# Kernel tuning notes

Hardware: AMD Instinct MI355X
Metric: run time of the kernel (lower is better)

The kernel has to match this reference:

```python
import jax, jax.numpy as jnp
import numpy as np

B, S, D, H = 2, 4096, 1024, 16
HD = D // H  # 64


def setup_inputs() -> dict:
    key = jax.random.key(0)
    ks = jax.random.split(key, 9)
    init = lambda k, shape: (jax.random.normal(k, shape, dtype=jnp.float32) * 0.02)
    return {
        "x": jax.random.normal(ks[0], (B, S, D), dtype=jnp.float32),
        "Wq": init(ks[1], (D, D)), "bq": init(ks[2], (D,)),
        "Wk": init(ks[3], (D, D)), "bk": init(ks[4], (D,)),
        "Wv": init(ks[5], (D, D)), "bv": init(ks[6], (D,)),
        "Wo": init(ks[7], (D, D)), "bo": init(ks[8], (D,)),
    }


def _split_heads(t):
    # [B, S, D] -> [B, H, S, HD]
    b, s, d = t.shape
    return t.reshape(b, s, H, HD).transpose(0, 2, 1, 3)


def reference(x, Wq, bq, Wk, bk, Wv, bv, Wo, bo):
    # q/k/v projections (torch Linear: x @ W.T + b)
    q = _split_heads(x @ Wq.T + bq)
    k = _split_heads(x @ Wk.T + bk)
    v = _split_heads(x @ Wv.T + bv)
    scale = 1.0 / np.sqrt(HD).astype(np.float32)
    # chunked_attention uses full K/V per chunk => equivalent to full attention.
    scores = jnp.einsum("bhqd,bhkd->bhqk", q, k) * scale
    # softmax computed in fp32 then cast back (matches F.softmax(dtype=float32))
    attn = jax.nn.softmax(scores.astype(jnp.float32), axis=-1).astype(scores.dtype)
    out = jnp.einsum("bhqk,bhkd->bhqd", attn, v)
    out = out.transpose(0, 2, 1, 3).reshape(B, S, D)  # combine heads
    return out @ Wo.T + bo
```

## Files before the change

### kernel.cpp

```cpp
#include <hip/hip_runtime.h>
#include <hip/hip_bf16.h>
#include <stdint.h>

typedef __attribute__((ext_vector_type(8))) short short8;
typedef __attribute__((ext_vector_type(4))) short short4v;
typedef __attribute__((ext_vector_type(4))) float f32x4;
typedef __attribute__((ext_vector_type(4))) unsigned int uint4v;

#define MFMA16(A, B, C) __builtin_amdgcn_mfma_f32_16x16x32_bf16(A, B, C, 0, 0, 0)

#define GLDS16(gp, lp) __builtin_amdgcn_global_load_lds(                     \
    (const __attribute__((address_space(1))) unsigned int*)(gp),             \
    (__attribute__((address_space(3))) unsigned int*)(lp), 16, 0, 0)

static constexpr int kS  = 4096;
static constexpr int kD  = 1024;
static constexpr int kH  = 16;
static constexpr int kHD = 64;

__device__ __forceinline__ short bf16_bits(float f) {
    __hip_bfloat16 h = __float2bfloat16(f);
    return *(short*)&h;
}

__device__ __forceinline__ unsigned int pk_bf16(float a, float b) {
    __hip_bfloat162 h = __float22bfloat162_rn(make_float2(a, b));
    return *(unsigned int*)&h;
}

__device__ __forceinline__ short8 cvt8(const float* __restrict__ p) {
    f32x4 a = ((const f32x4*)p)[0];
    f32x4 b = ((const f32x4*)p)[1];
    short8 r;
    r[0] = bf16_bits(a[0]); r[1] = bf16_bits(a[1]);
    r[2] = bf16_bits(a[2]); r[3] = bf16_bits(a[3]);
    r[4] = bf16_bits(b[0]); r[5] = bf16_bits(b[1]);
    r[6] = bf16_bits(b[2]); r[7] = bf16_bits(b[3]);
    return r;
}

__device__ __forceinline__ unsigned char f32_to_e4m3(float f) {
    unsigned int u = __float_as_uint(f);
    unsigned int s = (u >> 24) & 0x80u;
    unsigned int a = u & 0x7fffffffu;
    if (a < 0x3c800000u) {
        float af = __uint_as_float(a);
        unsigned int sub = (unsigned int)(af * 512.0f + 0.5f);
        return (unsigned char)(s | sub);
    }
    unsigned int r = a + 0x80000u;
    unsigned int m = (r >> 20) & 7u;
    int eb = (int)(r >> 23) - 127 + 7;
    unsigned int bits = ((unsigned int)eb << 3) | m;
    if (bits > 0x7Eu) bits = 0x7Eu;
    return (unsigned char)(s | bits);
}
__device__ __forceinline__ float e4m3_to_f32(unsigned int b) {
    unsigned int s = b & 0x80u;
    unsigned int e = (b >> 3) & 15u;
    unsigned int m = b & 7u;
    float f = e ? __uint_as_float(((e + 120u) << 23) | (m << 20))
                : (float)m * 0.001953125f;
    return s ? -f : f;
}

__global__ __launch_bounds__(256) void cvt_f32_bf16(
    const float* __restrict__ src, __hip_bfloat16* __restrict__ dst)
{
    const int i = blockIdx.x * 256 + threadIdx.x;
    f32x4 v = ((const f32x4*)src)[i];
    short4v o;
    o[0] = bf16_bits(v[0]); o[1] = bf16_bits(v[1]);
    o[2] = bf16_bits(v[2]); o[3] = bf16_bits(v[3]);
    ((short4v*)dst)[i] = o;
}

__global__ __launch_bounds__(256) void cvt_w4(
    const float* __restrict__ w0, const float* __restrict__ w1,
    const float* __restrict__ w2, const float* __restrict__ w3,
    __hip_bfloat16* __restrict__ dst)
{
    const int blk = blockIdx.x;
    const int sel = blk >> 10;
    const float* src = sel == 0 ? w0 : sel == 1 ? w1 : sel == 2 ? w2 : w3;
    const int i = (blk & 1023) * 256 + threadIdx.x;
    f32x4 v = ((const f32x4*)src)[i];
    short4v o;
    o[0] = bf16_bits(v[0]); o[1] = bf16_bits(v[1]);
    o[2] = bf16_bits(v[2]); o[3] = bf16_bits(v[3]);
    ((short4v*)(dst + (size_t)sel * kD * kD))[i] = o;
}

__global__ __launch_bounds__(256) void cvt_all(
    const float* __restrict__ x,
    const float* __restrict__ w0, const float* __restrict__ w1,
    const float* __restrict__ w2, const float* __restrict__ w3,
    __hip_bfloat16* __restrict__ xb, __hip_bfloat16* __restrict__ wdst)
{
    int blk = blockIdx.x;
    const float* src;
    __hip_bfloat16* dst;
    int i;
    if (blk < 8192) {
        src = x; dst = xb; i = blk * 256 + threadIdx.x;
    } else {
        blk -= 8192;
        const int sel = blk >> 10;
        src = sel == 0 ? w0 : sel == 1 ? w1 : sel == 2 ? w2 : w3;
        dst = wdst + (size_t)sel * kD * kD;
        i = (blk & 1023) * 256 + threadIdx.x;
    }
    f32x4 v = ((const f32x4*)src)[i];
    short4v o;
    o[0] = bf16_bits(v[0]); o[1] = bf16_bits(v[1]);
    o[2] = bf16_bits(v[2]); o[3] = bf16_bits(v[3]);
    ((short4v*)dst)[i] = o;
}


__global__ __launch_bounds__(256) void gemm_qkv(
    const __hip_bfloat16* __restrict__ X, const __hip_bfloat16* __restrict__ Wb,
    const float* __restrict__ bq, const float* __restrict__ bk,
    const float* __restrict__ bv,
    __hip_bfloat16* __restrict__ Qw, __hip_bfloat16* __restrict__ Kw,
    __hip_bfloat16* __restrict__ Vtw)
{
    __shared__ short As[128 * 64];
    __shared__ short Bs[128 * 64];

    const int lane = threadIdx.x & 63, wave = threadIdx.x >> 6;
    const int quad = lane >> 4, l16 = lane & 15;
    const int sel = blockIdx.y >> 3;
    const int m0 = blockIdx.x * 128, n0 = (blockIdx.y & 7) * 128;
    const int wm = wave & 1, wn = wave >> 1;

    const float* bias = sel == 0 ? bq : sel == 1 ? bk : bv;
    const short* Xg = (const short*)X + (size_t)m0 * kD;
    const short* Wg = (const short*)Wb + (size_t)sel * kD * kD + (size_t)n0 * kD;

    f32x4 acc[4][4];
    #pragma unroll
    for (int mt = 0; mt < 4; ++mt)
        #pragma unroll
        for (int nt = 0; nt < 4; ++nt) acc[mt][nt] = f32x4{0.f, 0.f, 0.f, 0.f};

    const int srow = lane >> 3;
    const int gch  = (lane & 7) ^ srow;

    for (int k0 = 0; k0 < kD; k0 += 64) {
        __syncthreads();
        #pragma unroll
        for (int i = 0; i < 4; ++i) {
            const int rowbase = wave * 32 + i * 8;
            const int row = rowbase + srow;
            GLDS16(Xg + (size_t)row * kD + k0 + gch * 8, &As[rowbase * 64]);
            GLDS16(Wg + (size_t)row * kD + k0 + gch * 8, &Bs[rowbase * 64]);
        }
        __syncthreads();

        #pragma unroll
        for (int c = 0; c < 2; ++c) {
            short8 af[4], bf[4];
            const int rx = l16 & 7;
            #pragma unroll
            for (int mt = 0; mt < 4; ++mt)
                af[mt] = *(const short8*)&As[(wm * 64 + mt * 16 + l16) * 64
                                             + (((c * 4 + quad) ^ rx) * 8)];
            #pragma unroll
            for (int nt = 0; nt < 4; ++nt)
                bf[nt] = *(const short8*)&Bs[(wn * 64 + nt * 16 + l16) * 64
                                             + (((c * 4 + quad) ^ rx) * 8)];
            #pragma unroll
            for (int mt = 0; mt < 4; ++mt)
                #pragma unroll
                for (int nt = 0; nt < 4; ++nt)
                    acc[mt][nt] = MFMA16(af[mt], bf[nt], acc[mt][nt]);
        }
    }

    #pragma unroll
    for (int nt = 0; nt < 4; ++nt) {
        const int n = n0 + wn * 64 + nt * 16 + l16;
        const float bvv = bias[n];
        #pragma unroll
        for (int mt = 0; mt < 4; ++mt) {
            if (sel == 2) {
                const int m = m0 + wm * 64 + mt * 16 + quad * 4;
                short4v pk;
                #pragma unroll
                for (int r = 0; r < 4; ++r)
                    pk[r] = bf16_bits(acc[mt][nt][r] + bvv);
                const int bh2 = (m >> 12) * kH + (n >> 6);
                short* dst = (short*)Vtw
                    + ((size_t)bh2 * kHD + (size_t)(n & (kHD - 1))) * kS
                    + (size_t)(m & (kS - 1));
                *(short4v*)dst = pk;
            } else {
                __hip_bfloat16* dst = sel == 0 ? Qw : Kw;
                const float scale = sel == 0 ? 0.18033688f : 1.0f;
                #pragma unroll
                for (int r = 0; r < 4; ++r) {
                    const int m = m0 + wm * 64 + mt * 16 + quad * 4 + r;
                    const float v = (acc[mt][nt][r] + bvv) * scale;
                    const size_t addr = (((size_t)(m >> 12) * kH + (n >> 6)) * kS
                                         + (size_t)(m & (kS - 1))) * kHD
                                        + (size_t)(n & (kHD - 1));
                    dst[addr] = __float2bfloat16(v);
                }
            }
        }
    }
}

__global__ __launch_bounds__(256) void gemm_out(
    const __hip_bfloat16* __restrict__ X, const __hip_bfloat16* __restrict__ W,
    const float* __restrict__ bias, float* __restrict__ out)
{
    __shared__ short As[128 * 64];
    __shared__ short Bs[128 * 64];

    const int lane = threadIdx.x & 63, wave = threadIdx.x >> 6;
    const int quad = lane >> 4, l16 = lane & 15;
    const int m0 = blockIdx.x * 128, n0 = blockIdx.y * 128;
    const int wm = wave & 1, wn = wave >> 1;

    const short* Xg = (const short*)X + (size_t)m0 * kD;
    const short* Wg = (const short*)W + (size_t)n0 * kD;

    f32x4 acc[4][4];
    #pragma unroll
    for (int mt = 0; mt < 4; ++mt)
        #pragma unroll
        for (int nt = 0; nt < 4; ++nt) acc[mt][nt] = f32x4{0.f, 0.f, 0.f, 0.f};

    const int srow = lane >> 3;
    const int gch  = (lane & 7) ^ srow;

    for (int k0 = 0; k0 < kD; k0 += 64) {
        __syncthreads();
        #pragma unroll
        for (int i = 0; i < 4; ++i) {
            const int rowbase = wave * 32 + i * 8;
            const int row = rowbase + srow;
            GLDS16(Xg + (size_t)row * kD + k0 + gch * 8, &As[rowbase * 64]);
            GLDS16(Wg + (size_t)row * kD + k0 + gch * 8, &Bs[rowbase * 64]);
        }
        __syncthreads();

        #pragma unroll
        for (int c = 0; c < 2; ++c) {
            short8 af[4], bf[4];
            const int rx = l16 & 7;
            #pragma unroll
            for (int mt = 0; mt < 4; ++mt)
                af[mt] = *(const short8*)&As[(wm * 64 + mt * 16 + l16) * 64
                                             + (((c * 4 + quad) ^ rx) * 8)];
            #pragma unroll
            for (int nt = 0; nt < 4; ++nt)
                bf[nt] = *(const short8*)&Bs[(wn * 64 + nt * 16 + l16) * 64
                                             + (((c * 4 + quad) ^ rx) * 8)];
            #pragma unroll
            for (int mt = 0; mt < 4; ++mt)
                #pragma unroll
                for (int nt = 0; nt < 4; ++nt)
                    acc[mt][nt] = MFMA16(af[mt], bf[nt], acc[mt][nt]);
        }
    }

    #pragma unroll
    for (int nt = 0; nt < 4; ++nt) {
        const int n = n0 + wn * 64 + nt * 16 + l16;
        const float bv = bias[n];
        #pragma unroll
        for (int mt = 0; mt < 4; ++mt)
            #pragma unroll
            for (int r = 0; r < 4; ++r) {
                const int m = m0 + wm * 64 + mt * 16 + quad * 4 + r;
                out[(size_t)m * kD + n] = acc[mt][nt][r] + bv;
            }
    }
}

__global__ __launch_bounds__(256, 2) void flash2(
    const __hip_bfloat16* __restrict__ Qw, const __hip_bfloat16* __restrict__ Kw,
    const __hip_bfloat16* __restrict__ Vt, __hip_bfloat16* __restrict__ O)
{
    __shared__ short Ks[2][8 * 512];
    __shared__ short Vs[2][8 * 512];

    const int lane = threadIdx.x & 63, wave = threadIdx.x >> 6;
    const int quad = lane >> 4, l16 = lane & 15;

    const int flat = blockIdx.y * 16 + blockIdx.x;
    const int swz  = (flat & 7) * 64 + (flat >> 3);
    const int bh = swz >> 4, b = bh >> 4, h = bh & 15;
    const int qbase = (swz & 15) * 256 + wave * 64;

    const short* Qg = (const short*)Qw + ((size_t)bh * kS + qbase) * kHD;
    short8 qf[4][2];
    #pragma unroll
    for (int t = 0; t < 4; ++t)
        #pragma unroll
        for (int c = 0; c < 2; ++c)
            qf[t][c] = *(const short8*)(Qg + (t * 16 + l16) * kHD + c * 32 + quad * 8);

    const short* Kg = (const short*)Kw + (size_t)bh * kS * kHD;
    const short* Vg = (const short*)Vt + (size_t)bh * kHD * kS;

    const short ONE = 0x3F80;
    const short8 onesf = {ONE, ONE, ONE, ONE, ONE, ONE, ONE, ONE};

    f32x4 o[4][4], lsumv[4];
    #pragma unroll
    for (int t = 0; t < 4; ++t) {
        lsumv[t] = f32x4{0.f, 0.f, 0.f, 0.f};
        #pragma unroll
        for (int dt = 0; dt < 4; ++dt) o[t][dt] = f32x4{0.f, 0.f, 0.f, 0.f};
    }

    const int kc = wave >> 1, km = wave & 1;
    const int krow = kc * 32 + 8 * (l16 >> 2) + 4 * km + (l16 & 3);
    const short* ka0 = Kg + (size_t)krow * kHD + quad * 8;
    const short* ka1 = ka0 + 32;
    const int vdt = (wave & 1) * 2, vc32 = (wave >> 1) * 32;
    const short* va0 = Vg + (size_t)((vdt + 0) * 16 + l16) * kS + vc32 + quad * 8;
    const short* va1 = Vg + (size_t)((vdt + 1) * 16 + l16) * kS + vc32 + quad * 8;

    GLDS16(ka0, &Ks[0][(wave * 2 + 0) * 512]);
    GLDS16(ka1, &Ks[0][(wave * 2 + 1) * 512]);
    GLDS16(va0, &Vs[0][(wave * 2 + 0) * 512]);
    GLDS16(va1, &Vs[0][(wave * 2 + 1) * 512]);
    ka0 += 64 * kHD; ka1 += 64 * kHD; va0 += 64; va1 += 64;

    for (int k0 = 0; k0 < kS; k0 += 64) {
        const int cur = (k0 >> 6) & 1;
        __syncthreads();
        if (k0 + 64 < kS) {
            const int nxt = cur ^ 1;
            GLDS16(ka0, &Ks[nxt][(wave * 2 + 0) * 512]);
            GLDS16(ka1, &Ks[nxt][(wave * 2 + 1) * 512]);
            GLDS16(va0, &Vs[nxt][(wave * 2 + 0) * 512]);
            GLDS16(va1, &Vs[nxt][(wave * 2 + 1) * 512]);
            ka0 += 64 * kHD; ka1 += 64 * kHD; va0 += 64; va1 += 64;
        }

        #pragma unroll
        for (int c = 0; c < 2; ++c) {
            short8 vb[4];
            #pragma unroll
            for (int dt = 0; dt < 4; ++dt)
                vb[dt] = *(const short8*)&Vs[cur][(c * 4 + dt) * 512 + lane * 8];

            unsigned int P[4][4];
            #pragma unroll
            for (int m = 0; m < 2; ++m) {
                const int fb = c * 4 + m * 2;
                short8 a0 = *(const short8*)&Ks[cur][(fb + 0) * 512 + lane * 8];
                short8 a1 = *(const short8*)&Ks[cur][(fb + 1) * 512 + lane * 8];
                #pragma unroll
                for (int t = 0; t < 4; ++t) {
                    f32x4 z = {0.f, 0.f, 0.f, 0.f};
                    f32x4 s = MFMA16(a0, qf[t][0], z);
                    s = MFMA16(a1, qf[t][1], s);
                    P[t][m * 2 + 0] = pk_bf16(__builtin_amdgcn_exp2f(s[0]),
                                              __builtin_amdgcn_exp2f(s[1]));
                    P[t][m * 2 + 1] = pk_bf16(__builtin_amdgcn_exp2f(s[2]),
                                              __builtin_amdgcn_exp2f(s[3]));
                }
            }

            short8 pa[4];
            #pragma unroll
            for (int t = 0; t < 4; ++t) {
                uint4v u = {P[t][0], P[t][1], P[t][2], P[t][3]};
                pa[t] = __builtin_bit_cast(short8, u);
            }

            __builtin_amdgcn_s_setprio(1);
            #pragma unroll
            for (int t = 0; t < 4; ++t)
                lsumv[t] = MFMA16(pa[t], onesf, lsumv[t]);
            #pragma unroll
            for (int dt = 0; dt < 4; ++dt)
                #pragma unroll
                for (int t = 0; t < 4; ++t)
                    o[t][dt] = MFMA16(pa[t], vb[dt], o[t][dt]);
            __builtin_amdgcn_s_setprio(0);
        }
    }

    #pragma unroll
    for (int t = 0; t < 4; ++t)
        #pragma unroll
        for (int r = 0; r < 4; ++r) {
            const float inv = 1.0f / lsumv[t][r];
            const int sq = qbase + t * 16 + quad * 4 + r;
            #pragma unroll
            for (int dt = 0; dt < 4; ++dt)
                O[((size_t)b * kS + sq) * kD + h * kHD + dt * 16 + l16] =
                    __float2bfloat16(o[t][dt][r] * inv);
        }
}

template <bool KV8, bool WB16>
__global__ __launch_bounds__(256) void gemm_kv(
    const float* __restrict__ X, const void* __restrict__ W,
    const float* __restrict__ bias, void* __restrict__ outv)
{
    const int lane = threadIdx.x & 63;
    const int wave = threadIdx.x >> 6;
    const int quad = lane >> 4;
    const int l16  = lane & 15;
    const int m0 = blockIdx.x * 16;
    const int n0 = blockIdx.y * 256 + wave * 64;

    const float* xr = X + (size_t)(m0 + l16) * kD;
    const float* wf = (const float*)W + (size_t)(n0 + l16) * kD;
    const short* wb = (const short*)W + (size_t)(n0 + l16) * kD;

    f32x4 acc[4] = {{0.f,0.f,0.f,0.f},{0.f,0.f,0.f,0.f},
                    {0.f,0.f,0.f,0.f},{0.f,0.f,0.f,0.f}};

    for (int k8 = quad; k8 < kD / 8; k8 += 4) {
        short8 a = cvt8(xr + k8 * 8);
        #pragma unroll
        for (int nt = 0; nt < 4; ++nt) {
            short8 w = WB16 ? *(const short8*)(wb + nt * 16 * kD + k8 * 8)
                            : cvt8(wf + nt * 16 * kD + k8 * 8);
            acc[nt] = MFMA16(a, w, acc[nt]);
        }
    }

    #pragma unroll
    for (int nt = 0; nt < 4; ++nt) {
        const int n = n0 + nt * 16 + l16;
        const float bv = bias[n];
        #pragma unroll
        for (int r = 0; r < 4; ++r) {
            const int m = m0 + quad * 4 + r;
            const float v = acc[nt][r] + bv;
            const size_t addr = (((size_t)(m >> 12) * kH + (n >> 6)) * kS
                                 + (size_t)(m & (kS - 1))) * kHD + (size_t)(n & (kHD - 1));
            if (KV8) ((unsigned char*)outv)[addr] = f32_to_e4m3(v);
            else     ((__hip_bfloat16*)outv)[addr] = __float2bfloat16(v);
        }
    }
}

template <bool KV8, bool WB16>
__global__ __launch_bounds__(256) void flash_fusedq(
    const float* __restrict__ x,  const void* __restrict__ Wq,
    const float* __restrict__ bq, const void* __restrict__ Kw,
    const void* __restrict__ Vw,  __hip_bfloat16* __restrict__ O)
{
    __shared__ short pool[9216];
    __shared__ short Ps[4][32][72];

    const int lane = threadIdx.x & 63;
    const int wave = threadIdx.x >> 6;
    const int quad = lane >> 4;
    const int l16  = lane & 15;
    const int bh   = blockIdx.y;
    const int b    = bh >> 4, h = bh & 15;
    const int qbase = blockIdx.x * 128 + wave * 32;

    {
        const float* xr0 = x + (size_t)(b * kS + qbase + l16) * kD;
        const float* xr1 = xr0 + (size_t)16 * kD;
        const float* wqf = (const float*)Wq + (size_t)(h * kHD + l16) * kD;
        const short* wqb = (const short*)Wq + (size_t)(h * kHD + l16) * kD;
        f32x4 qa[2][4];
        #pragma unroll
        for (int t = 0; t < 2; ++t)
            #pragma unroll
            for (int nt = 0; nt < 4; ++nt) qa[t][nt] = f32x4{0.f,0.f,0.f,0.f};

        for (int k8 = quad; k8 < kD / 8; k8 += 4) {
            short8 a0 = cvt8(xr0 + k8 * 8);
            short8 a1 = cvt8(xr1 + k8 * 8);
            #pragma unroll
            for (int nt = 0; nt < 4; ++nt) {
                short8 w = WB16 ? *(const short8*)(wqb + nt * 16 * kD + k8 * 8)
                                : cvt8(wqf + nt * 16 * kD + k8 * 8);
                qa[0][nt] = MFMA16(a0, w, qa[0][nt]);
                qa[1][nt] = MFMA16(a1, w, qa[1][nt]);
            }
        }
        #pragma unroll
        for (int t = 0; t < 2; ++t)
            #pragma unroll
            for (int nt = 0; nt < 4; ++nt) {
                const float bv = bq[h * kHD + nt * 16 + l16];
                #pragma unroll
                for (int r = 0; r < 4; ++r)
                    pool[wave * 2304 + (t * 16 + quad * 4 + r) * 72 + nt * 16 + l16] =
                        bf16_bits((qa[t][nt][r] + bv) * 0.125f);
            }
    }
    short8 qf[2][2];
    #pragma unroll
    for (int t = 0; t < 2; ++t)
        #pragma unroll
        for (int c = 0; c < 2; ++c)
            qf[t][c] = *(const short8*)&pool[wave * 2304 + (t * 16 + l16) * 72 + c * 32 + quad * 8];

    f32x4 o[2][4];
    float mrow[2][4], lrow[2][4];
    #pragma unroll
    for (int t = 0; t < 2; ++t)
        #pragma unroll
        for (int dt = 0; dt < 4; ++dt) o[t][dt] = f32x4{0.f,0.f,0.f,0.f};
    #pragma unroll
    for (int t = 0; t < 2; ++t)
        #pragma unroll
        for (int r = 0; r < 4; ++r) { mrow[t][r] = -INFINITY; lrow[t][r] = 0.f; }

    const __hip_bfloat16* Kb16 = (const __hip_bfloat16*)Kw + (size_t)bh * kS * kHD;
    const __hip_bfloat16* Vb16 = (const __hip_bfloat16*)Vw + (size_t)bh * kS * kHD;
    const unsigned char*  K8   = (const unsigned char*)Kw + (size_t)bh * kS * kHD;
    const unsigned char*  V8   = (const unsigned char*)Vw + (size_t)bh * kS * kHD;

    for (int k0 = 0; k0 < kS; k0 += 64) {
        __syncthreads();
        #pragma unroll
        for (int i = 0; i < 2; ++i) {
            const int lin = threadIdx.x + i * 256;
            const int kr = lin >> 3, c8 = lin & 7;
            short8 kv, vv;
            if (KV8) {
                uint2 kbits = *(const uint2*)(K8 + (size_t)(k0 + kr) * kHD + c8 * 8);
                uint2 vbits = *(const uint2*)(V8 + (size_t)(k0 + kr) * kHD + c8 * 8);
                #pragma unroll
                for (int j = 0; j < 4; ++j) {
                    kv[j]     = bf16_bits(e4m3_to_f32((kbits.x >> (8 * j)) & 255u));
                    kv[4 + j] = bf16_bits(e4m3_to_f32((kbits.y >> (8 * j)) & 255u));
                    vv[j]     = bf16_bits(e4m3_to_f32((vbits.x >> (8 * j)) & 255u));
                    vv[4 + j] = bf16_bits(e4m3_to_f32((vbits.y >> (8 * j)) & 255u));
                }
            } else {
                kv = *(const short8*)(Kb16 + (size_t)(k0 + kr) * kHD + c8 * 8);
                vv = *(const short8*)(Vb16 + (size_t)(k0 + kr) * kHD + c8 * 8);
            }
            *(short8*)&pool[kr * 72 + c8 * 8] = kv;
            #pragma unroll
            for (int j = 0; j < 8; ++j)
                pool[4608 + (c8 * 8 + j) * 72 + (((kr >> 3) ^ c8) << 3) + (kr & 7)] = vv[j];
        }
        __syncthreads();

        f32x4 sc[2][4];
        #pragma unroll
        for (int kt = 0; kt < 4; ++kt) {
            short8 b0 = *(const short8*)&pool[(kt * 16 + l16) * 72 + quad * 8];
            short8 b1 = *(const short8*)&pool[(kt * 16 + l16) * 72 + 32 + quad * 8];
            f32x4 z = {0.f, 0.f, 0.f, 0.f};
            f32x4 s0 = MFMA16(qf[0][0], b0, z); s0 = MFMA16(qf[0][1], b1, s0);
            f32x4 s1 = MFMA16(qf[1][0], b0, z); s1 = MFMA16(qf[1][1], b1, s1);
            sc[0][kt] = s0; sc[1][kt] = s1;
        }

        #pragma unroll
        for (int t = 0; t < 2; ++t)
            #pragma unroll
            for (int r = 0; r < 4; ++r) {
                float s0 = sc[t][0][r], s1 = sc[t][1][r];
                float s2 = sc[t][2][r], s3 = sc[t][3][r];
                float mx = fmaxf(fmaxf(s0, s1), fmaxf(s2, s3));
                #pragma unroll
                for (int off = 1; off < 16; off <<= 1)
                    mx = fmaxf(mx, __shfl_xor(mx, off, 64));
                const float mnew  = fmaxf(mrow[t][r], mx);
                const float alpha = __builtin_amdgcn_exp2f((mrow[t][r] - mnew) * 1.44269504f);
                mrow[t][r] = mnew;
                const float p0 = __builtin_amdgcn_exp2f((s0 - mnew) * 1.44269504f);
                const float p1 = __builtin_amdgcn_exp2f((s1 - mnew) * 1.44269504f);
                const float p2 = __builtin_amdgcn_exp2f((s2 - mnew) * 1.44269504f);
                const float p3 = __builtin_amdgcn_exp2f((s3 - mnew) * 1.44269504f);
                float ps = (p0 + p1) + (p2 + p3);
                #pragma unroll
                for (int off = 1; off < 16; off <<= 1)
                    ps += __shfl_xor(ps, off, 64);
                lrow[t][r] = lrow[t][r] * alpha + ps;
                o[t][0][r] *= alpha; o[t][1][r] *= alpha;
                o[t][2][r] *= alpha; o[t][3][r] *= alpha;
                const int row = t * 16 + quad * 4 + r;
                Ps[wave][row][l16]      = bf16_bits(p0);
                Ps[wave][row][16 + l16] = bf16_bits(p1);
                Ps[wave][row][32 + l16] = bf16_bits(p2);
                Ps[wave][row][48 + l16] = bf16_bits(p3);
            }

        short8 pa[2][2];
        #pragma unroll
        for (int t = 0; t < 2; ++t)
            #pragma unroll
            for (int c = 0; c < 2; ++c)
                pa[t][c] = *(const short8*)&Ps[wave][t * 16 + l16][c * 32 + quad * 8];
        #pragma unroll
        for (int c = 0; c < 2; ++c)
            #pragma unroll
            for (int dt = 0; dt < 4; ++dt) {
                const int d = dt * 16 + l16;
                short8 vb = *(const short8*)&pool[4608 + d * 72 + ((((c * 4 + quad)) ^ (d >> 3)) << 3)];
                o[0][dt] = MFMA16(pa[0][c], vb, o[0][dt]);
                o[1][dt] = MFMA16(pa[1][c], vb, o[1][dt]);
            }
    }

    #pragma unroll
    for (int t = 0; t < 2; ++t)
        #pragma unroll
        for (int r = 0; r < 4; ++r) {
            const float inv = 1.0f / lrow[t][r];
            const int sq = qbase + t * 16 + quad * 4 + r;
            #pragma unroll
            for (int dt = 0; dt < 4; ++dt)
                O[((size_t)b * kS + sq) * kD + h * kHD + dt * 16 + l16] =
                    __float2bfloat16(o[t][dt][r] * inv);
        }
}

template <bool WB16>
__global__ __launch_bounds__(256) void proj_out(
    const __hip_bfloat16* __restrict__ Xb, const void* __restrict__ W,
    const float* __restrict__ bias, float* __restrict__ out)
{
    const int lane = threadIdx.x & 63;
    const int wave = threadIdx.x >> 6;
    const int quad = lane >> 4;
    const int l16  = lane & 15;
    const int m0 = blockIdx.x * 16;
    const int n0 = blockIdx.y * 256 + wave * 64;

    const short8* xr = (const short8*)((const short*)Xb + (size_t)(m0 + l16) * kD);
    const float*  wf = (const float*)W + (size_t)(n0 + l16) * kD;
    const short*  wb = (const short*)W + (size_t)(n0 + l16) * kD;

    f32x4 acc[4] = {{0.f,0.f,0.f,0.f},{0.f,0.f,0.f,0.f},
                    {0.f,0.f,0.f,0.f},{0.f,0.f,0.f,0.f}};

    for (int k8 = quad; k8 < kD / 8; k8 += 4) {
        short8 a = xr[k8];
        #pragma unroll
        for (int nt = 0; nt < 4; ++nt) {
            short8 w = WB16 ? *(const short8*)(wb + nt * 16 * kD + k8 * 8)
                            : cvt8(wf + nt * 16 * kD + k8 * 8);
            acc[nt] = MFMA16(a, w, acc[nt]);
        }
    }

    #pragma unroll
    for (int nt = 0; nt < 4; ++nt) {
        const int n = n0 + nt * 16 + l16;
        const float bv = bias[n];
        #pragma unroll
        for (int r = 0; r < 4; ++r) {
            const int m = m0 + quad * 4 + r;
            out[(size_t)m * kD + n] = acc[nt][r] + bv;
        }
    }
}

extern "C" void kernel_launch(void* const* d_in, const int* in_sizes, int n_in,
                              void* d_out, int out_size, void* d_ws, size_t ws_size,
                              hipStream_t stream)
{
    const float* x = nullptr;
    const float* Wm[4] = {nullptr, nullptr, nullptr, nullptr};
    const float* bm[4] = {nullptr, nullptr, nullptr, nullptr};
    int wi = 0, bi = 0;
    for (int i = 0; i < n_in; ++i) {
        const int s = in_sizes[i];
        if      (s == 2 * kS * kD)         x = (const float*)d_in[i];
        else if (s == kD * kD && wi < 4)   Wm[wi++] = (const float*)d_in[i];
        else if (s == kD      && bi < 4)   bm[bi++] = (const float*)d_in[i];
    }
    const float *Wq = Wm[0], *Wk = Wm[1], *Wv = Wm[2], *Wo = Wm[3];
    const float *bq = bm[0], *bk = bm[1], *bv = bm[2], *bo = bm[3];
    float* out = (float*)d_out;

    const size_t elems = (size_t)2 * kS * kD;
    const size_t wel   = (size_t)kD * kD;
    const size_t MB = 1024 * 1024;
    dim3 bb(256);

    if (ws_size >= 88 * MB) {
        __hip_bfloat16* xb  = (__hip_bfloat16*)d_ws;
        __hip_bfloat16* Qw  = xb + elems;
        __hip_bfloat16* Kw  = Qw + elems;
        __hip_bfloat16* Vtw = Kw + elems;
        __hip_bfloat16* Ow  = Vtw + elems;
        __hip_bfloat16* Wqb = Ow + elems;
        __hip_bfloat16* Wob = Wqb + 3 * wel;

        cvt_all<<<dim3(12288), bb, 0, stream>>>(x, Wq, Wk, Wv, Wo, xb, Wqb);

        gemm_qkv<<<dim3(64, 24), bb, 0, stream>>>(xb, Wqb, bq, bk, bv, Qw, Kw, Vtw);
        flash2<<<dim3(16, 32), bb, 0, stream>>>(Qw, Kw, Vtw, Ow);
        gemm_out<<<dim3(64, 8), bb, 0, stream>>>(Ow, Wob, bo, out);
        return;
    }

    dim3 gg(512, 4), gf(kS / 128, 2 * kH);
    if (ws_size >= 56 * MB) {
        __hip_bfloat16* Kw  = (__hip_bfloat16*)d_ws;
        __hip_bfloat16* Vw  = Kw + elems;
        __hip_bfloat16* Ow  = Vw + elems;
        __hip_bfloat16* Wqb = Ow + elems;
        __hip_bfloat16* Wkb = Wqb + wel;
        __hip_bfloat16* Wvb = Wkb + wel;
        __hip_bfloat16* Wob = Wvb + wel;
        cvt_w4<<<dim3(4096), bb, 0, stream>>>(Wq, Wk, Wv, Wo, Wqb);
        gemm_kv<false, true><<<gg, bb, 0, stream>>>(x, Wkb, bk, Kw);
        gemm_kv<false, true><<<gg, bb, 0, stream>>>(x, Wvb, bv, Vw);
        flash_fusedq<false, true><<<gf, bb, 0, stream>>>(x, Wqb, bq, Kw, Vw, Ow);
        proj_out<true><<<gg, bb, 0, stream>>>(Ow, Wob, bo, out);
    } else if (ws_size >= 48 * MB) {
        __hip_bfloat16* Kw = (__hip_bfloat16*)d_ws;
        __hip_bfloat16* Vw = Kw + elems;
        __hip_bfloat16* Ow = Vw + elems;
        gemm_kv<false, false><<<gg, bb, 0, stream>>>(x, Wk, bk, Kw);
        gemm_kv<false, false><<<gg, bb, 0, stream>>>(x, Wv, bv, Vw);
        flash_fusedq<false, false><<<gf, bb, 0, stream>>>(x, Wq, bq, Kw, Vw, Ow);
        proj_out<false><<<gg, bb, 0, stream>>>(Ow, Wo, bo, out);
    } else {
        unsigned char* Kw = (unsigned char*)d_ws;
        unsigned char* Vw = Kw + elems;
        __hip_bfloat16* Ow = (__hip_bfloat16*)(Vw + elems);
        gemm_kv<true, false><<<gg, bb, 0, stream>>>(x, Wk, bk, Kw);
        gemm_kv<true, false><<<gg, bb, 0, stream>>>(x, Wv, bv, Vw);
        flash_fusedq<true, false><<<gf, bb, 0, stream>>>(x, Wq, bq, Kw, Vw, Ow);
        proj_out<false><<<gg, bb, 0, stream>>>(Ow, Wo, bo, out);
    }
}
```

Before: 345.0 us.

## Double KV tile to 128 and replace row-sum MFMA with VALU accumulation

The flash attention kernel now stages 128 keys per iteration instead of 64, with each wave issuing four async global-to-LDS loads per tile. This halves the number of barriers and loop iterations per key sweep. The softmax denominator is now summed in fp32 on the vector ALU and reduced across lanes with shuffles at the end, instead of a ones-vector MFMA per tile. LDS use doubles to 64KB per block, which may limit the two-blocks-per-CU occupancy, and the row sum now uses fp32 exp values rather than the bf16-rounded P.

```diff
diff --git a/kernel.cpp b/kernel.cpp
--- a/kernel.cpp
+++ b/kernel.cpp
@@ -285,8 +285,8 @@
     const __hip_bfloat16* __restrict__ Qw, const __hip_bfloat16* __restrict__ Kw,
     const __hip_bfloat16* __restrict__ Vt, __hip_bfloat16* __restrict__ O)
 {
-    __shared__ short Ks[2][8 * 512];
-    __shared__ short Vs[2][8 * 512];
+    __shared__ short Ks[2][16 * 512];
+    __shared__ short Vs[2][16 * 512];
 
     const int lane = threadIdx.x & 63, wave = threadIdx.x >> 6;
     const int quad = lane >> 4, l16 = lane & 15;
@@ -307,45 +307,41 @@
     const short* Kg = (const short*)Kw + (size_t)bh * kS * kHD;
     const short* Vg = (const short*)Vt + (size_t)bh * kHD * kS;
 
-    const short ONE = 0x3F80;
-    const short8 onesf = {ONE, ONE, ONE, ONE, ONE, ONE, ONE, ONE};
-
-    f32x4 o[4][4], lsumv[4];
-    #pragma unroll
-    for (int t = 0; t < 4; ++t) {
-        lsumv[t] = f32x4{0.f, 0.f, 0.f, 0.f};
+    f32x4 o[4][4];
+    float psum[4] = {0.f, 0.f, 0.f, 0.f};
+    #pragma unroll
+    for (int t = 0; t < 4; ++t)
         #pragma unroll
         for (int dt = 0; dt < 4; ++dt) o[t][dt] = f32x4{0.f, 0.f, 0.f, 0.f};
-    }
-
-    const int kc = wave >> 1, km = wave & 1;
-    const int krow = kc * 32 + 8 * (l16 >> 2) + 4 * km + (l16 & 3);
-    const short* ka0 = Kg + (size_t)krow * kHD + quad * 8;
-    const short* ka1 = ka0 + 32;
-    const int vdt = (wave & 1) * 2, vc32 = (wave >> 1) * 32;
-    const short* va0 = Vg + (size_t)((vdt + 0) * 16 + l16) * kS + vc32 + quad * 8;
-    const short* va1 = Vg + (size_t)((vdt + 1) * 16 + l16) * kS + vc32 + quad * 8;
-
-    GLDS16(ka0, &Ks[0][(wave * 2 + 0) * 512]);
-    GLDS16(ka1, &Ks[0][(wave * 2 + 1) * 512]);
-    GLDS16(va0, &Vs[0][(wave * 2 + 0) * 512]);
-    GLDS16(va1, &Vs[0][(wave * 2 + 1) * 512]);
-    ka0 += 64 * kHD; ka1 += 64 * kHD; va0 += 64; va1 += 64;
-
-    for (int k0 = 0; k0 < kS; k0 += 64) {
-        const int cur = (k0 >> 6) & 1;
+
+    const short* ka = Kg + (size_t)(wave * 32 + 8 * (l16 >> 2) + (l16 & 3)) * kHD
+                    + quad * 8;
+    const short* va = Vg + (size_t)l16 * kS + wave * 32 + quad * 8;
+
+    #pragma unroll
+    for (int i = 0; i < 4; ++i) {
+        GLDS16(ka + (size_t)((i >> 1) * 4) * kHD + (i & 1) * 32,
+               &Ks[0][(wave * 4 + i) * 512]);
+        GLDS16(va + (size_t)(i * 16) * kS, &Vs[0][(wave * 4 + i) * 512]);
+    }
+    ka += 128 * kHD; va += 128;
+
+    for (int k0 = 0; k0 < kS; k0 += 128) {
+        const int cur = (k0 >> 7) & 1;
         __syncthreads();
-        if (k0 + 64 < kS) {
+        if (k0 + 128 < kS) {
             const int nxt = cur ^ 1;
-            GLDS16(ka0, &Ks[nxt][(wave * 2 + 0) * 512]);
-            GLDS16(ka1, &Ks[nxt][(wave * 2 + 1) * 512]);
-            GLDS16(va0, &Vs[nxt][(wave * 2 + 0) * 512]);
-            GLDS16(va1, &Vs[nxt][(wave * 2 + 1) * 512]);
-            ka0 += 64 * kHD; ka1 += 64 * kHD; va0 += 64; va1 += 64;
-        }
-
-        #pragma unroll
-        for (int c = 0; c < 2; ++c) {
+            #pragma unroll
+            for (int i = 0; i < 4; ++i) {
+                GLDS16(ka + (size_t)((i >> 1) * 4) * kHD + (i & 1) * 32,
+                       &Ks[nxt][(wave * 4 + i) * 512]);
+                GLDS16(va + (size_t)(i * 16) * kS, &Vs[nxt][(wave * 4 + i) * 512]);
+            }
+            ka += 128 * kHD; va += 128;
+        }
+
+        #pragma unroll
+        for (int c = 0; c < 4; ++c) {
             short8 vb[4];
             #pragma unroll
             for (int dt = 0; dt < 4; ++dt)
@@ -362,10 +358,13 @@
                     f32x4 z = {0.f, 0.f, 0.f, 0.f};
                     f32x4 s = MFMA16(a0, qf[t][0], z);
                     s = MFMA16(a1, qf[t][1], s);
-                    P[t][m * 2 + 0] = pk_bf16(__builtin_amdgcn_exp2f(s[0]),
-                                              __builtin_amdgcn_exp2f(s[1]));
-                    P[t][m * 2 + 1] = pk_bf16(__builtin_amdgcn_exp2f(s[2]),
-                                              __builtin_amdgcn_exp2f(s[3]));
+                    const float e0 = __builtin_amdgcn_exp2f(s[0]);
+                    const float e1 = __builtin_amdgcn_exp2f(s[1]);
+                    const float e2 = __builtin_amdgcn_exp2f(s[2]);
+                    const float e3 = __builtin_amdgcn_exp2f(s[3]);
+                    psum[t] += (e0 + e1) + (e2 + e3);
+                    P[t][m * 2 + 0] = pk_bf16(e0, e1);
+                    P[t][m * 2 + 1] = pk_bf16(e2, e3);
                 }
             }
 
@@ -378,9 +377,6 @@
 
             __builtin_amdgcn_s_setprio(1);
             #pragma unroll
-            for (int t = 0; t < 4; ++t)
-                lsumv[t] = MFMA16(pa[t], onesf, lsumv[t]);
-            #pragma unroll
             for (int dt = 0; dt < 4; ++dt)
                 #pragma unroll
                 for (int t = 0; t < 4; ++t)
@@ -390,16 +386,21 @@
     }
 
     #pragma unroll
-    for (int t = 0; t < 4; ++t)
+    for (int t = 0; t < 4; ++t) {
+        float L = psum[t];
+        L += __shfl_xor(L, 16, 64);
+        L += __shfl_xor(L, 32, 64);
         #pragma unroll
         for (int r = 0; r < 4; ++r) {
-            const float inv = 1.0f / lsumv[t][r];
+            const float Lr = __shfl(L, quad * 4 + r, 64);
+            const float inv = 1.0f / Lr;
             const int sq = qbase + t * 16 + quad * 4 + r;
             #pragma unroll
             for (int dt = 0; dt < 4; ++dt)
                 O[((size_t)b * kS + sq) * kD + h * kHD + dt * 16 + l16] =
                     __float2bfloat16(o[t][dt][r] * inv);
         }
+    }
 }
 
 template <bool KV8, bool WB16>
```

Result: slower. 359.6 us (+4.2%).
